# Performance work log

Measured on AMD Instinct MI355X. Metric: run time of the kernel, lower is better.

## Reference

```python
import jax, jax.numpy as jnp
import numpy as np

NUM_CLASSES = 3
IMG = 448
STRIDES = (8, 16, 32)
POS_IOU, NEG_IOU = 0.5, 0.3
NEG_RATIO = 3
B, T = 64, 20


def _make_anchors(stride):
    f = IMG // stride
    cs = (np.arange(f, dtype=np.float32) + 0.5) * stride
    cx, cy = np.meshgrid(cs, cs, indexing='xy')            # [f, f]
    sizes = np.array([2.0, 2.5, 3.0], np.float32) * stride  # 3 square anchors / loc
    cx = np.broadcast_to(cx[..., None], (f, f, 3))
    cy = np.broadcast_to(cy[..., None], (f, f, 3))
    w = np.broadcast_to(sizes, (f, f, 3))
    boxes = np.stack([cx - w / 2, cy - w / 2, cx + w / 2, cy + w / 2], -1)
    return jnp.asarray(boxes.reshape(-1, 4), jnp.float32)   # [f*f*3, 4]


def setup_inputs() -> dict:
    key = jax.random.key(0)
    k1, k2, k3, kc, ks, kl = jax.random.split(key, 6)
    pred1 = jax.random.normal(k1, (B, 24, 56, 56), jnp.float32)
    pred2 = jax.random.normal(k2, (B, 24, 28, 28), jnp.float32)
    pred3 = jax.random.normal(k3, (B, 24, 14, 14), jnp.float32)
    ctr = jax.random.uniform(kc, (B, T, 2), jnp.float32, 20.0, IMG - 20.0)
    wh = jax.random.uniform(ks, (B, T, 2), jnp.float32, 20.0, 120.0)
    target_boxes = jnp.concatenate([ctr - wh / 2, ctr + wh / 2], axis=-1)  # [B,T,4] xyxy
    target_labels = jax.random.randint(kl, (B, T), 1, NUM_CLASSES + 1, jnp.int32)
    return {
        'pred1': pred1, 'pred2': pred2, 'pred3': pred3,
        'anchor1': _make_anchors(8), 'anchor2': _make_anchors(16), 'anchor3': _make_anchors(32),
        'target_boxes': target_boxes, 'target_labels': target_labels,
    }


def _iou(a, b):  # a [A,4], b [T,4] -> [A,T]
    lt = jnp.maximum(a[:, None, :2], b[None, :, :2])
    rb = jnp.minimum(a[:, None, 2:], b[None, :, 2:])
    wh = jnp.clip(rb - lt, 0.0)
    inter = wh[..., 0] * wh[..., 1]
    area_a = (a[:, 2] - a[:, 0]) * (a[:, 3] - a[:, 1])
    area_b = (b[:, 2] - b[:, 0]) * (b[:, 3] - b[:, 1])
    return inter / (area_a[:, None] + area_b[None, :] - inter + 1e-9)


def _encode(gt, an):  # both [A,4] xyxy -> [A,4] deltas
    aw, ah = an[:, 2] - an[:, 0], an[:, 3] - an[:, 1]
    acx, acy = (an[:, 0] + an[:, 2]) * 0.5, (an[:, 1] + an[:, 3]) * 0.5
    gw, gh = gt[:, 2] - gt[:, 0], gt[:, 3] - gt[:, 1]
    gcx, gcy = (gt[:, 0] + gt[:, 2]) * 0.5, (gt[:, 1] + gt[:, 3]) * 0.5
    return jnp.stack([(gcx - acx) / aw, (gcy - acy) / ah,
                      jnp.log(gw / aw), jnp.log(gh / ah)], axis=-1)


def _bce_logits(x, y):
    return jnp.maximum(x, 0.0) - x * y + jnp.log1p(jnp.exp(-jnp.abs(x)))


def _image_loss(deltas, obj, cls, boxes, labels, anchors):
    # deltas [A,4], obj [A], cls [A,K], boxes [T,4], labels [T], anchors [A,4]
    iou = _iou(anchors, boxes)                    # [A,T]
    matched_t = jnp.argmax(iou, axis=1)           # [A]
    max_iou = jnp.max(iou, axis=1)
    pos = max_iou >= POS_IOU
    neg = max_iou < NEG_IOU
    # force each GT's best anchor to be positive
    best_a = jnp.argmax(iou, axis=0)              # [T]
    matched_t = matched_t.at[best_a].set(jnp.arange(boxes.shape[0]))
    pos = pos.at[best_a].set(True)
    neg = neg.at[best_a].set(False)
    matched_labels = jnp.where(pos, labels[matched_t], 0)
    # objectness + hard negative mining (rank-based topk, jit-safe)
    obj_t = (matched_labels > 0).astype(obj.dtype)
    bce = _bce_logits(obj, obj_t)
    num_pos = pos.sum()
    need = jnp.minimum(NEG_RATIO * num_pos, neg.sum())
    rank = jnp.argsort(jnp.argsort(-jnp.where(neg, bce, -jnp.inf)))
    sel = pos | ((rank < need) & neg)
    obj_loss = jnp.sum(jnp.where(sel, bce, 0.0)) / jnp.maximum(sel.sum(), 1)
    # classification (mean over positives)
    logp = jax.nn.log_softmax(cls, axis=-1)
    tgt = jnp.maximum(matched_labels - 1, 0)
    ce = -jnp.take_along_axis(logp, tgt[:, None], axis=1)[:, 0]
    cls_loss = jnp.sum(jnp.where(pos, ce, 0.0)) / jnp.maximum(num_pos, 1)
    # localization: smooth L1, mean over positive anchor elements
    tdel = _encode(boxes[matched_t], anchors)
    d = jnp.abs(deltas - tdel)
    sl1 = jnp.where(d < 1.0, 0.5 * d * d, d - 0.5)
    loc_loss = jnp.sum(jnp.where(pos[:, None], sl1, 0.0)) / jnp.maximum(4 * num_pos, 1)
    return obj_loss, cls_loss, loc_loss


def _scale_loss(pred, anchors, boxes, labels):
    Bp, C, H, W = pred.shape
    p = pred.transpose(0, 2, 3, 1).reshape(Bp, H * W * 3, 5 + NUM_CLASSES)
    deltas, obj, cls = p[..., :4], p[..., 4], p[..., 5:]
    fn = jax.vmap(lambda d, o, c, b, l: _image_loss(d, o, c, b, l, anchors))
    ol, cl, ll = fn(deltas, obj, cls, boxes, labels)
    return ol.sum(), cl.sum(), ll.sum()


def reference(pred1, pred2, pred3, anchor1, anchor2, anchor3, target_boxes, target_labels):
    tot = jnp.zeros(3, jnp.float32)
    for pred, anc in ((pred1, anchor1), (pred2, anchor2), (pred3, anchor3)):
        ol, cl, ll = _scale_loss(pred, anc, target_boxes, target_labels)
        tot = tot + jnp.stack([ol, cl, ll])
    bsz = target_boxes.shape[0]
    obj, cls, loc = tot[0] / bsz, tot[1] / bsz, tot[2] / bsz
    total = obj + cls + 2.0 * loc
    return jnp.stack([obj, cls, loc, total])
```

## Files before the change

kernel.cpp:

```cpp
#include <hip/hip_runtime.h>
#include <math.h>

#define T 20
#define MAXA 9408
#define LOSS_OFF 16

static __device__ __forceinline__ unsigned mapf(float x) {
    unsigned u = __float_as_uint(x);
    return (u & 0x80000000u) ? ~u : (u | 0x80000000u);
}
static __device__ __forceinline__ float unmapf(unsigned m) {
    return __uint_as_float((m & 0x80000000u) ? (m ^ 0x80000000u) : ~m);
}
static __device__ __forceinline__ float bce_pos(float x) {
    return fmaxf(x, 0.f) - x + log1pf(expf(-fabsf(x)));
}
static __device__ __forceinline__ float bce_neg(float x) {
    return fmaxf(x, 0.f) + log1pf(expf(-fabsf(x)));
}

__global__ __launch_bounds__(1024, 1) void fused_kernel(
    const float* __restrict__ pred1, const float* __restrict__ pred2,
    const float* __restrict__ pred3, const float* __restrict__ tboxes,
    const int* __restrict__ tlabels, float* __restrict__ wsf)
{
#pragma clang fp contract(off)
    const int bid = blockIdx.x;
    const int b = bid / 3, s = bid - 3 * b;
    const float* __restrict__ pred = (s == 0) ? pred1 : (s == 1) ? pred2 : pred3;
    const int W = 56 >> s, HW = W * W, A = 3 * HW;
    const float stf = (float)(8 << s);
    const int sh = 3 - s;

    __shared__ unsigned       s_key[MAXA];
    __shared__ unsigned short s_mf[MAXA];
    __shared__ float4   s_box[T];
    __shared__ float    s_ab[T];
    __shared__ int      s_lab[T];
    __shared__ int      s_besta[T];
    __shared__ unsigned whist[4][256];
    __shared__ unsigned s_npnn;
    __shared__ unsigned s_bc[2];
    __shared__ float    s_redf[16 * 4];

    const int tid = threadIdx.x, lane = tid & 63, wid = tid >> 6;

    if (tid < T) {
        float4 g = ((const float4*)tboxes)[b * T + tid];
        s_box[tid] = g;
        s_ab[tid]  = (g.z - g.x) * (g.w - g.y);
        s_lab[tid] = tlabels[b * T + tid];
    }
    if (tid == 0) s_npnn = 0u;
    __syncthreads();

    const float* objbase = pred + (size_t)(b * 24 + 4) * HW;

    for (int j0 = 4 * tid; j0 < A; j0 += 4096) {
        float ax[4], ay[4], az[4], aw[4], ar[4], bn[4], bu[4];
        int at_[4];
        float xlo = 1e30f, xhi = -1e30f, ylo = 1e30f, yhi = -1e30f;
#pragma unroll
        for (int r = 0; r < 4; r++) {
            int j = j0 + r;
            int k   = (j >= HW) + (j >= 2 * HW);
            int pix = j - k * HW;
            int qq  = pix >> sh;
            int py  = (qq * 9363) >> 16;
            int px  = pix - py * W;
            float w  = (2.0f + 0.5f * (float)k) * stf;
            float cx = ((float)px + 0.5f) * stf;
            float cy = ((float)py + 0.5f) * stf;
            ax[r] = cx - 0.5f * w; ay[r] = cy - 0.5f * w;
            az[r] = cx + 0.5f * w; aw[r] = cy + 0.5f * w;
            ar[r] = w * w;
            bn[r] = 0.f; bu[r] = 1.f; at_[r] = 0;
            xlo = fminf(xlo, ax[r]); xhi = fmaxf(xhi, az[r]);
            ylo = fminf(ylo, ay[r]); yhi = fmaxf(yhi, aw[r]);
        }
        for (int t = 0; t < T; t++) {
            float4 g = s_box[t];
            if (g.x < xhi && g.z > xlo && g.y < yhi && g.w > ylo) {
                float ab = s_ab[t];
#pragma unroll
                for (int r = 0; r < 4; r++) {
                    float lx = fmaxf(ax[r], g.x), ly = fmaxf(ay[r], g.y);
                    float rx = fminf(az[r], g.z), ry = fminf(aw[r], g.w);
                    float ww = fmaxf(rx - lx, 0.f), hh = fmaxf(ry - ly, 0.f);
                    float inter = ww * hh;
                    float u = ((ar[r] + ab) - inter) + 1e-9f;
                    if (inter * bu[r] > bn[r] * u) {
                        bn[r] = inter; bu[r] = u; at_[r] = t;
                    }
                }
            }
        }
#pragma unroll
        for (int r = 0; r < 4; r++) {
            int j = j0 + r;
            int k   = (j >= HW) + (j >= 2 * HW);
            int pix = j - k * HW;
            bool pos = (bn[r] + bn[r] >= bu[r]);
            bool neg = (bn[r] < 0.3f * bu[r]);
            unsigned key = 0u;
            if (neg) key = mapf(objbase[(size_t)k * 8 * HW + pix]);
            s_key[j] = key;
            s_mf[j]  = (unsigned short)(at_[r] | (pos ? 0x100 : 0) | (neg ? 0x200 : 0));
        }
    }

    for (int t = wid; t < T; t += 16) {
        float4 g = s_box[t];
        float  ab = s_ab[t];
        int px0 = max(0, (int)floorf(g.x / stf) - 2);
        int px1 = min(W - 1, (int)floorf(g.z / stf) + 2);
        int py0 = max(0, (int)floorf(g.y / stf) - 2);
        int py1 = min(W - 1, (int)floorf(g.w / stf) + 2);
        int rowlen = (px1 - px0 + 1) * 3;
        float bi = -1.f, bu2 = 1.f;
        int ba = 0;
        for (int py = py0; py <= py1; py++) {
            float cy = ((float)py + 0.5f) * stf;
            for (int cc = lane; cc < rowlen; cc += 64) {
                int ix = (cc * 21846) >> 16;
                int k  = cc - 3 * ix;
                int px = px0 + ix;
                float w  = (2.0f + 0.5f * (float)k) * stf;
                float cx = ((float)px + 0.5f) * stf;
                float lx = fmaxf(cx - 0.5f * w, g.x), ly = fmaxf(cy - 0.5f * w, g.y);
                float rx = fminf(cx + 0.5f * w, g.z), ry = fminf(cy + 0.5f * w, g.w);
                float ww = fmaxf(rx - lx, 0.f), hh = fmaxf(ry - ly, 0.f);
                float inter = ww * hh;
                float u = ((w * w + ab) - inter) + 1e-9f;
                if (inter * bu2 > bi * u) {
                    bi = inter; bu2 = u; ba = (py * W + px) * 3 + k;
                }
            }
        }
        for (int off = 32; off; off >>= 1) {
            float oi = __shfl_down(bi, off, 64);
            float ou = __shfl_down(bu2, off, 64);
            int   oa = __shfl_down(ba, off, 64);
            float l = oi * bu2, r = bi * ou;
            if (l > r || (l == r && oa < ba)) { bi = oi; bu2 = ou; ba = oa; }
        }
        if (lane == 0) {
            int pix = (ba * 21846) >> 16;
            int k = ba - 3 * pix;
            s_besta[t] = k * HW + pix;
        }
    }
    __syncthreads();

    if (tid < T) {
        int j20 = s_besta[tid];
        bool winner = true;
        for (int t2 = tid + 1; t2 < T; t2++) if (s_besta[t2] == j20) winner = false;
        if (winner) {
            s_mf[j20]  = (unsigned short)(tid | 0x100);
            s_key[j20] = 0u;
        }
    }
    __syncthreads();

    unsigned npnn = 0;
    for (int j = tid; j < A; j += 1024) {
        unsigned m = s_mf[j];
        npnn += ((m >> 8) & 1u) + (((m >> 9) & 1u) << 16);
    }
    for (int off = 32; off; off >>= 1) npnn += (unsigned)__shfl_down((int)npnn, off, 64);
    if (lane == 0) atomicAdd(&s_npnn, npnn);
    __syncthreads();
    unsigned np = s_npnn & 0xFFFFu, nn = s_npnn >> 16;
    unsigned need = min(3u * np, nn);

    unsigned kth = 0xFFFFFFFFu;
    if (need > 0) {
        unsigned prefix = 0, remaining = need;
        for (int p = 0; p < 4; p++) {
            const int sh_ = 24 - 8 * p;
            (&whist[0][0])[tid] = 0u;
            __syncthreads();
            for (int j = tid; j < A; j += 1024) {
                unsigned k = s_key[j];
                bool ok = (p == 0) || ((k >> (sh_ + 8)) == prefix);
                if (ok) atomicAdd(&whist[wid >> 2][(k >> sh_) & 255u], 1u);
            }
            __syncthreads();
            if (tid < 256) {
                whist[0][tid] = whist[0][tid] + whist[1][tid]
                              + whist[2][tid] + whist[3][tid];
            }
            __syncthreads();
            if (wid == 0) {
                int b0 = lane * 4;
                unsigned csum = whist[0][b0] + whist[0][b0 + 1]
                              + whist[0][b0 + 2] + whist[0][b0 + 3];
                unsigned Tv = csum;
                for (int off = 1; off < 64; off <<= 1) {
                    unsigned o = __shfl_down(Tv, off, 64);
                    if (lane + off < 64) Tv += o;
                }
                unsigned long long ball = __ballot(Tv >= remaining);
                int L = 63 - __clzll(ball);
                if (lane == L) {
                    unsigned sv = Tv - csum;
                    int bb = b0 + 3;
                    while (true) { sv += whist[0][bb]; if (sv >= remaining) break; bb--; }
                    s_bc[0] = (unsigned)bb;
                    s_bc[1] = sv - whist[0][bb];
                }
            }
            __syncthreads();
            remaining -= s_bc[1];
            prefix = (prefix << 8) | s_bc[0];
            __syncthreads();
        }
        kth = prefix;
    }

    float obj_s = 0.f, cls_s = 0.f, loc_s = 0.f;
    unsigned cgt = 0;
    for (int j = tid; j < A; j += 1024) {
        unsigned mfv = s_mf[j];
        if (mfv & 0x100u) {
            int k   = (j >= HW) + (j >= 2 * HW);
            int pix = j - k * HW;
            const float* bp = pred + (size_t)(b * 24 + k * 8) * HW + pix;
            float x = bp[(size_t)4 * HW];
            obj_s += bce_pos(x);
            int t = mfv & 0xFFu;
            float4 g = s_box[t];
            int tgt = s_lab[t] - 1;
            float c0 = bp[(size_t)5 * HW], c1 = bp[(size_t)6 * HW], c2 = bp[(size_t)7 * HW];
            float mm  = fmaxf(c0, fmaxf(c1, c2));
            float lse = logf(expf(c0 - mm) + expf(c1 - mm) + expf(c2 - mm));
            float ct = (tgt == 0) ? c0 : (tgt == 1) ? c1 : c2;
            cls_s += (mm + lse) - ct;
            int qq = pix >> sh;
            int py = (qq * 9363) >> 16;
            int px = pix - py * W;
            float w  = (2.0f + 0.5f * (float)k) * stf;
            float cx = ((float)px + 0.5f) * stf;
            float cy = ((float)py + 0.5f) * stf;
            float gcx = (g.x + g.z) * 0.5f, gcy = (g.y + g.w) * 0.5f;
            float gw = g.z - g.x, gh = g.w - g.y;
            float t0 = (gcx - cx) / w, t1 = (gcy - cy) / w;
            float t2 = logf(gw / w),   t3 = logf(gh / w);
            float d0 = bp[0], d1 = bp[(size_t)HW], d2 = bp[(size_t)2 * HW], d3 = bp[(size_t)3 * HW];
            float dd;
            dd = fabsf(d0 - t0); loc_s += (dd < 1.f) ? 0.5f * dd * dd : dd - 0.5f;
            dd = fabsf(d1 - t1); loc_s += (dd < 1.f) ? 0.5f * dd * dd : dd - 0.5f;
            dd = fabsf(d2 - t2); loc_s += (dd < 1.f) ? 0.5f * dd * dd : dd - 0.5f;
            dd = fabsf(d3 - t3); loc_s += (dd < 1.f) ? 0.5f * dd * dd : dd - 0.5f;
        } else {
            unsigned key = s_key[j];
            if (key > kth) { obj_s += bce_neg(unmapf(key)); cgt++; }
        }
    }
    for (int off = 32; off; off >>= 1) {
        obj_s += __shfl_down(obj_s, off, 64);
        cls_s += __shfl_down(cls_s, off, 64);
        loc_s += __shfl_down(loc_s, off, 64);
        cgt   += (unsigned)__shfl_down((int)cgt, off, 64);
    }
    if (lane == 0) {
        s_redf[wid * 4 + 0] = obj_s;
        s_redf[wid * 4 + 1] = cls_s;
        s_redf[wid * 4 + 2] = loc_s;
        s_redf[wid * 4 + 3] = __uint_as_float(cgt);
    }
    __syncthreads();
    if (tid == 0) {
        float ob = 0.f, cl = 0.f, lc = 0.f;
        unsigned cg = 0;
        for (int w2 = 0; w2 < 16; w2++) {
            ob += s_redf[w2 * 4 + 0];
            cl += s_redf[w2 * 4 + 1];
            lc += s_redf[w2 * 4 + 2];
            cg += __float_as_uint(s_redf[w2 * 4 + 3]);
        }
        if (need > 0) ob += (float)(need - cg) * bce_neg(unmapf(kth));
        wsf[LOSS_OFF + bid * 3 + 0] = ob / (float)max(np + need, 1u);
        wsf[LOSS_OFF + bid * 3 + 1] = cl / (float)max(np, 1u);
        wsf[LOSS_OFF + bid * 3 + 2] = lc / (float)max(4u * np, 1u);
    }
}

__global__ void finalize_kernel(const float* __restrict__ wsf,
                                float* __restrict__ out) {
    const int t = threadIdx.x, lane = t & 63, wid = t >> 6;
    __shared__ float red[12];
    float v0 = 0.f, v1 = 0.f, v2 = 0.f;
    if (t < 192) {
        v0 = wsf[LOSS_OFF + 3 * t];
        v1 = wsf[LOSS_OFF + 3 * t + 1];
        v2 = wsf[LOSS_OFF + 3 * t + 2];
    }
    for (int off = 32; off; off >>= 1) {
        v0 += __shfl_down(v0, off, 64);
        v1 += __shfl_down(v1, off, 64);
        v2 += __shfl_down(v2, off, 64);
    }
    if (lane == 0) { red[wid * 3] = v0; red[wid * 3 + 1] = v1; red[wid * 3 + 2] = v2; }
    __syncthreads();
    if (t == 0) {
        float obj = 0.f, cls = 0.f, loc = 0.f;
        for (int w2 = 0; w2 < 4; w2++) {
            obj += red[w2 * 3]; cls += red[w2 * 3 + 1]; loc += red[w2 * 3 + 2];
        }
        obj /= 64.f; cls /= 64.f; loc /= 64.f;
        out[0] = obj; out[1] = cls; out[2] = loc;
        out[3] = obj + cls + 2.f * loc;
    }
}

extern "C" void kernel_launch(void* const* d_in, const int* in_sizes, int n_in,
                              void* d_out, int out_size, void* d_ws, size_t ws_size,
                              hipStream_t stream) {
    const float* pred1   = (const float*)d_in[0];
    const float* pred2   = (const float*)d_in[1];
    const float* pred3   = (const float*)d_in[2];
    const float* tboxes  = (const float*)d_in[6];
    const int*   tlabels = (const int*)d_in[7];
    float* wsf = (float*)d_ws;
    float* out = (float*)d_out;

    fused_kernel<<<64 * 3, 1024, 0, stream>>>(
        pred1, pred2, pred3, tboxes, tlabels, wsf);
    finalize_kernel<<<1, 256, 0, stream>>>(wsf, out);
}
```

Measured before the change: 116.9 us.

## Restructure hard-negative radix select to 3 passes and fold pos/neg counting into IoU loop

Switches the radix select for the k-th negative key from four 8-bit passes with per-wave sub-histograms to three 11/11/10-bit passes on a single shared histogram. Positive and negative counts are now gathered during the IoU pass and corrected for forced best-anchor assignments with an atomic adjustment, which removes a separate counting sweep and a barrier. Objectness loads are hoisted ahead of the IoU loop as contiguous loads, and the match-flag array shrinks to bytes. The trade-off is more contention on one histogram and a longer per-lane bucket scan in the prefix search.

After: 115.8 us. About the same (-0.9%).

```diff
diff --git a/kernel.cpp b/kernel.cpp
--- a/kernel.cpp
+++ b/kernel.cpp
@@ -18,6 +18,7 @@
 static __device__ __forceinline__ float bce_neg(float x) {
     return fmaxf(x, 0.f) + log1pf(expf(-fabsf(x)));
 }
+
 
 __global__ __launch_bounds__(1024, 1) void fused_kernel(
     const float* __restrict__ pred1, const float* __restrict__ pred2,
@@ -32,14 +33,14 @@
     const float stf = (float)(8 << s);
     const int sh = 3 - s;
 
-    __shared__ unsigned       s_key[MAXA];
-    __shared__ unsigned short s_mf[MAXA];
+    __shared__ unsigned      s_key[MAXA];
+    __shared__ unsigned char s_mf[MAXA];
+    __shared__ unsigned      hist[2048];
     __shared__ float4   s_box[T];
     __shared__ float    s_ab[T];
     __shared__ int      s_lab[T];
     __shared__ int      s_besta[T];
-    __shared__ unsigned whist[4][256];
-    __shared__ unsigned s_npnn;
+    __shared__ unsigned s_npnn, s_adj;
     __shared__ unsigned s_bc[2];
     __shared__ float    s_redf[16 * 4];
 
@@ -51,20 +52,24 @@
         s_ab[tid]  = (g.z - g.x) * (g.w - g.y);
         s_lab[tid] = tlabels[b * T + tid];
     }
-    if (tid == 0) s_npnn = 0u;
+    if (tid == 0) { s_npnn = 0u; s_adj = 0u; }
     __syncthreads();
 
     const float* objbase = pred + (size_t)(b * 24 + 4) * HW;
 
+    unsigned npnn = 0;
     for (int j0 = 4 * tid; j0 < A; j0 += 4096) {
+        int k    = (j0 >= HW) + (j0 >= 2 * HW);
+        int pix0 = j0 - k * HW;
+        const float* op = objbase + (size_t)k * 8 * HW + pix0;
+        float xo0 = op[0], xo1 = op[1], xo2 = op[2], xo3 = op[3];
+
         float ax[4], ay[4], az[4], aw[4], ar[4], bn[4], bu[4];
         int at_[4];
         float xlo = 1e30f, xhi = -1e30f, ylo = 1e30f, yhi = -1e30f;
 #pragma unroll
         for (int r = 0; r < 4; r++) {
-            int j = j0 + r;
-            int k   = (j >= HW) + (j >= 2 * HW);
-            int pix = j - k * HW;
+            int pix = pix0 + r;
             int qq  = pix >> sh;
             int py  = (qq * 9363) >> 16;
             int px  = pix - py * W;
@@ -95,19 +100,19 @@
                 }
             }
         }
+        float xo[4] = {xo0, xo1, xo2, xo3};
 #pragma unroll
         for (int r = 0; r < 4; r++) {
             int j = j0 + r;
-            int k   = (j >= HW) + (j >= 2 * HW);
-            int pix = j - k * HW;
             bool pos = (bn[r] + bn[r] >= bu[r]);
             bool neg = (bn[r] < 0.3f * bu[r]);
-            unsigned key = 0u;
-            if (neg) key = mapf(objbase[(size_t)k * 8 * HW + pix]);
-            s_key[j] = key;
-            s_mf[j]  = (unsigned short)(at_[r] | (pos ? 0x100 : 0) | (neg ? 0x200 : 0));
-        }
-    }
+            s_key[j] = neg ? mapf(xo[r]) : 0u;
+            s_mf[j]  = (unsigned char)(at_[r] | (pos ? 0x20 : 0) | (neg ? 0x40 : 0));
+            npnn += (pos ? 1u : 0u) + (neg ? 0x10000u : 0u);
+        }
+    }
+    for (int off = 32; off; off >>= 1) npnn += (unsigned)__shfl_down((int)npnn, off, 64);
+    if (lane == 0) atomicAdd(&s_npnn, npnn);
 
     for (int t = wid; t < T; t += 16) {
         float4 g = s_box[t];
@@ -152,50 +157,52 @@
     }
     __syncthreads();
 
+    int  j20 = 0; bool winner = false;
     if (tid < T) {
-        int j20 = s_besta[tid];
-        bool winner = true;
-        for (int t2 = tid + 1; t2 < T; t2++) if (s_besta[t2] == j20) winner = false;
-        if (winner) {
-            s_mf[j20]  = (unsigned short)(tid | 0x100);
-            s_key[j20] = 0u;
-        }
-    }
-    __syncthreads();
-
-    unsigned npnn = 0;
-    for (int j = tid; j < A; j += 1024) {
-        unsigned m = s_mf[j];
-        npnn += ((m >> 8) & 1u) + (((m >> 9) & 1u) << 16);
-    }
-    for (int off = 32; off; off >>= 1) npnn += (unsigned)__shfl_down((int)npnn, off, 64);
-    if (lane == 0) atomicAdd(&s_npnn, npnn);
-    __syncthreads();
-    unsigned np = s_npnn & 0xFFFFu, nn = s_npnn >> 16;
+        int a = s_besta[tid];
+        j20 = a;
+        winner = true; bool first = true;
+        for (int t2 = tid + 1; t2 < T; t2++) if (s_besta[t2] == a) winner = false;
+        for (int t2 = 0; t2 < tid; t2++)     if (s_besta[t2] == a) first  = false;
+        if (first) {
+            unsigned old = s_mf[a];
+            unsigned d = ((old & 0x20u) ? 0u : 1u) +
+                         ((old & 0x40u) ? 0xFFFF0000u : 0u);
+            atomicAdd(&s_adj, d);
+        }
+    }
+    hist[tid] = 0u; hist[tid + 1024] = 0u;
+    __syncthreads();
+
+    if (tid < T && winner) {
+        s_mf[j20]  = (unsigned char)(tid | 0x20);
+        s_key[j20] = 0u;
+    }
+    __syncthreads();
+
+    unsigned packed = s_npnn + s_adj;
+    unsigned np = packed & 0xFFFFu, nn = packed >> 16;
     unsigned need = min(3u * np, nn);
 
     unsigned kth = 0xFFFFFFFFu;
     if (need > 0) {
         unsigned prefix = 0, remaining = need;
-        for (int p = 0; p < 4; p++) {
-            const int sh_ = 24 - 8 * p;
-            (&whist[0][0])[tid] = 0u;
-            __syncthreads();
+        const int shifts[3] = {21, 10, 0};
+        const int nbits[3]  = {11, 11, 10};
+        for (int p = 0; p < 3; p++) {
+            const int NB = 1 << nbits[p];
+            const int sh_ = shifts[p];
             for (int j = tid; j < A; j += 1024) {
                 unsigned k = s_key[j];
-                bool ok = (p == 0) || ((k >> (sh_ + 8)) == prefix);
-                if (ok) atomicAdd(&whist[wid >> 2][(k >> sh_) & 255u], 1u);
-            }
-            __syncthreads();
-            if (tid < 256) {
-                whist[0][tid] = whist[0][tid] + whist[1][tid]
-                              + whist[2][tid] + whist[3][tid];
+                bool ok = (p == 0) || ((k >> (sh_ + nbits[p])) == prefix);
+                if (ok) atomicAdd(&hist[(k >> sh_) & (NB - 1)], 1u);
             }
             __syncthreads();
             if (wid == 0) {
-                int b0 = lane * 4;
-                unsigned csum = whist[0][b0] + whist[0][b0 + 1]
-                              + whist[0][b0 + 2] + whist[0][b0 + 3];
+                const int C = NB >> 6;
+                int b0 = lane * C;
+                unsigned csum = 0;
+                for (int i = 0; i < C; i++) csum += hist[b0 + i];
                 unsigned Tv = csum;
                 for (int off = 1; off < 64; off <<= 1) {
                     unsigned o = __shfl_down(Tv, off, 64);
@@ -205,15 +212,16 @@
                 int L = 63 - __clzll(ball);
                 if (lane == L) {
                     unsigned sv = Tv - csum;
-                    int bb = b0 + 3;
-                    while (true) { sv += whist[0][bb]; if (sv >= remaining) break; bb--; }
+                    int bb = b0 + C - 1;
+                    while (true) { sv += hist[bb]; if (sv >= remaining) break; bb--; }
                     s_bc[0] = (unsigned)bb;
-                    s_bc[1] = sv - whist[0][bb];
+                    s_bc[1] = sv - hist[bb];
                 }
             }
             __syncthreads();
             remaining -= s_bc[1];
-            prefix = (prefix << 8) | s_bc[0];
+            prefix = (prefix << nbits[p]) | s_bc[0];
+            if (p < 2) { hist[tid] = 0u; hist[tid + 1024] = 0u; }
             __syncthreads();
         }
         kth = prefix;
@@ -223,13 +231,13 @@
     unsigned cgt = 0;
     for (int j = tid; j < A; j += 1024) {
         unsigned mfv = s_mf[j];
-        if (mfv & 0x100u) {
+        if (mfv & 0x20u) {
             int k   = (j >= HW) + (j >= 2 * HW);
             int pix = j - k * HW;
             const float* bp = pred + (size_t)(b * 24 + k * 8) * HW + pix;
             float x = bp[(size_t)4 * HW];
             obj_s += bce_pos(x);
-            int t = mfv & 0xFFu;
+            int t = mfv & 0x1Fu;
             float4 g = s_box[t];
             int tgt = s_lab[t] - 1;
             float c0 = bp[(size_t)5 * HW], c1 = bp[(size_t)6 * HW], c2 = bp[(size_t)7 * HW];
```
